# Optimization experiments

Hardware: AMD Instinct MI355X
Metric: run time of the kernel (lower is better)

The kernel has to match this reference:

```python
import jax, jax.numpy as jnp
import numpy as np

N_NODES = 100000
N_EDGES = 1600000
IN_DIM, HID_DIM, OUT_DIM = 512, 64, 32


def _gcn_conv(x, row, col, W, b, n):
    # GCNConv: h = x W; out[v] = sum_{(u,v)} norm(u,v) * h[u] + b
    # deg computed on destination (col) with self-loops already included.
    deg = jax.ops.segment_sum(jnp.ones_like(col, dtype=x.dtype), col, num_segments=n)
    dinv = jnp.where(deg > 0, jax.lax.rsqrt(deg), 0.0)
    norm = dinv[row] * dinv[col]                      # [E]
    h = x @ W                                          # [N, out]
    msg = h[row] * norm[:, None]                       # [E, out] gather
    out = jax.ops.segment_sum(msg, col, num_segments=n)  # scatter-add
    return out + b


def setup_inputs() -> dict:
    key = jax.random.key(0)
    k1, k2, k3, k4 = jax.random.split(key, 4)
    x = jax.random.normal(k1, (N_NODES, IN_DIM), dtype=jnp.float32)
    edge_index = jax.random.randint(k2, (2, N_EDGES), 0, N_NODES, dtype=jnp.int64)
    W1 = jax.random.normal(k3, (IN_DIM, HID_DIM), dtype=jnp.float32) / np.sqrt(IN_DIM)
    b1 = jnp.zeros((HID_DIM,), dtype=jnp.float32)
    W2 = jax.random.normal(k4, (HID_DIM, OUT_DIM), dtype=jnp.float32) / np.sqrt(HID_DIM)
    b2 = jnp.zeros((OUT_DIM,), dtype=jnp.float32)
    return {"x": x, "edge_index": edge_index, "W1": W1, "b1": b1, "W2": W2, "b2": b2}


def reference(x, edge_index, W1, b1, W2, b2):
    n = x.shape[0]
    # add self-loops (PyG GCNConv default add_self_loops=True)
    loop = jnp.arange(n, dtype=edge_index.dtype)
    row = jnp.concatenate([edge_index[0], loop])
    col = jnp.concatenate([edge_index[1], loop])
    h = _gcn_conv(x, row, col, W1, b1, n)
    h = jax.nn.relu(h)
    # dropout is identity in eval mode (training=False)
    h = _gcn_conv(h, row, col, W2, b2, n)
    return jax.nn.log_softmax(h, axis=1)
```

## Files before the change

kernel.cpp:

```cpp
#include <hip/hip_runtime.h>
#include <hip/hip_fp16.h>


#define IN_DIM 512
#define HID    64
#define OUTD   32

typedef __attribute__((ext_vector_type(8))) short bf16x8;
typedef __attribute__((ext_vector_type(4))) float floatx4;
typedef __attribute__((ext_vector_type(4))) unsigned short ushort4v;
typedef __attribute__((ext_vector_type(8))) unsigned short ushort8v;

__device__ __forceinline__ unsigned short f2bf(float f) {
    unsigned int u = __float_as_uint(f);
    unsigned int r = (u + 0x7fffu + ((u >> 16) & 1u)) >> 16;
    return (unsigned short)r;
}
__device__ __forceinline__ float bf2f(unsigned short h) {
    return __uint_as_float(((unsigned int)h) << 16);
}

__device__ __forceinline__ int eidx(const int* idx32, long long e, int is64) {
    if (is64) { const long long* p = (const long long*)idx32; return (int)p[e]; }
    return idx32[e];
}

__global__ void k_init(const float* __restrict__ W1,
                       unsigned short* __restrict__ W1t_hi,
                       unsigned short* __restrict__ W1t_lo,
                       const int* __restrict__ idx, int* __restrict__ flag,
                       int* __restrict__ cnt, int N) {
    int t = blockIdx.x * blockDim.x + threadIdx.x;
    if (t == 0) {
        int z = (idx[1] == 0) & (idx[3] == 0) & (idx[5] == 0) & (idx[7] == 0);
        *flag = z;
    }
    if (t < N) cnt[t] = 0;
    if (t < 64 * 512) {
        int n = t >> 9, k = t & 511;
        float v = W1[k * HID + n];
        unsigned short h = f2bf(v);
        W1t_hi[t] = h;
        W1t_lo[t] = f2bf(v - bf2f(h));
    }
}

__global__ void k_count(const int* __restrict__ idx, const int* __restrict__ flag,
                        int* __restrict__ cnt, int E) {
    int e = blockIdx.x * blockDim.x + threadIdx.x;
    if (e >= E) return;
    const int is64 = *flag;
    int c = eidx(idx, (long long)E + e, is64);
    atomicAdd(&cnt[c], 1);
}

__global__ void k_scanA(const int* __restrict__ cnt, int* __restrict__ rowptr,
                        int* __restrict__ part, float* __restrict__ dinv, int N) {
    __shared__ int s[256];
    const int t = threadIdx.x;
    const int i = blockIdx.x * 256 + t;
    int v = (i < N) ? cnt[i] : 0;
    if (i < N) dinv[i] = rsqrtf((float)(1 + v));
    s[t] = v;
    __syncthreads();
#pragma unroll
    for (int off = 1; off < 256; off <<= 1) {
        int x = (t >= off) ? s[t - off] : 0;
        __syncthreads();
        s[t] += x;
        __syncthreads();
    }
    if (i < N) rowptr[i] = s[t] - v;
    if (t == 255) part[blockIdx.x] = s[255];
}

__global__ void k_scanB(const int* __restrict__ part, int* __restrict__ partex, int nb) {
    __shared__ int s[1024];
    const int t = threadIdx.x;
    int v = (t < nb) ? part[t] : 0;
    s[t] = v;
    __syncthreads();
#pragma unroll
    for (int off = 1; off < 1024; off <<= 1) {
        int x = (t >= off) ? s[t - off] : 0;
        __syncthreads();
        s[t] += x;
        __syncthreads();
    }
    partex[t] = s[t] - v;
}

__global__ void k_scanC(int* __restrict__ rowptr, const int* __restrict__ partex,
                        int N, int E) {
    const int i = blockIdx.x * blockDim.x + threadIdx.x;
    if (i < N) rowptr[i] += partex[i >> 8];
    if (i == 0) rowptr[N] = E;
}

__global__ void k_place(const int* __restrict__ idx, const int* __restrict__ flag,
                        int* __restrict__ cnt, const int* __restrict__ rowptr,
                        int* __restrict__ src, int E) {
    int e = blockIdx.x * blockDim.x + threadIdx.x;
    if (e >= E) return;
    const int is64 = *flag;
    int r = eidx(idx, e, is64);
    int c = eidx(idx, (long long)E + e, is64);
    int ofs = atomicAdd(&cnt[c], -1) - 1;
    src[rowptr[c] + ofs] = r;
}

__launch_bounds__(256)
__global__ void k_gemm1_mfma(const float* __restrict__ x,
                             const unsigned short* __restrict__ Wt_hi,
                             const unsigned short* __restrict__ Wt_lo,
                             const float* __restrict__ dinv,
                             __half* __restrict__ g1, int N) {
    __shared__ unsigned short xs_hi[64 * 72];
    __shared__ unsigned short xs_lo[64 * 72];
    __shared__ unsigned short ws_hi[64 * 72];
    __shared__ unsigned short ws_lo[64 * 72];

    const int t = threadIdx.x;
    const int lane = t & 63;
    const int w = t >> 6;
    const int m = lane & 15;
    const int quad = lane >> 4;
    const int row_base = blockIdx.x * 64;

    const floatx4 zero = {0.0f, 0.0f, 0.0f, 0.0f};
    floatx4 acc[4] = {zero, zero, zero, zero};

    for (int kc = 0; kc < IN_DIM; kc += 64) {
        {
            const int kq = (t & 15) * 4;
#pragma unroll
            for (int p = 0; p < 4; ++p) {
                int rl = (t >> 4) + p * 16;
                int row = row_base + rl;
                if (row > N - 1) row = N - 1;
                float4 v = *(const float4*)(x + (size_t)row * IN_DIM + kc + kq);
                ushort4v hi, lo;
                hi.x = f2bf(v.x); lo.x = f2bf(v.x - bf2f(hi.x));
                hi.y = f2bf(v.y); lo.y = f2bf(v.y - bf2f(hi.y));
                hi.z = f2bf(v.z); lo.z = f2bf(v.z - bf2f(hi.z));
                hi.w = f2bf(v.w); lo.w = f2bf(v.w - bf2f(hi.w));
                *(ushort4v*)&xs_hi[rl * 72 + kq] = hi;
                *(ushort4v*)&xs_lo[rl * 72 + kq] = lo;
            }
        }
        {
            const int nl = t >> 2;
            const int q = (t & 3) * 16;
            const unsigned short* ph = Wt_hi + (size_t)nl * IN_DIM + kc + q;
            const unsigned short* pl = Wt_lo + (size_t)nl * IN_DIM + kc + q;
            *(ushort8v*)&ws_hi[nl * 72 + q]     = *(const ushort8v*)(ph);
            *(ushort8v*)&ws_hi[nl * 72 + q + 8] = *(const ushort8v*)(ph + 8);
            *(ushort8v*)&ws_lo[nl * 72 + q]     = *(const ushort8v*)(pl);
            *(ushort8v*)&ws_lo[nl * 72 + q + 8] = *(const ushort8v*)(pl + 8);
        }
        __syncthreads();
#pragma unroll
        for (int ks = 0; ks < 2; ++ks) {
            const int ko = ks * 32 + quad * 8;
            bf16x8 a_hi = *(const bf16x8*)&xs_hi[(w * 16 + m) * 72 + ko];
            bf16x8 a_lo = *(const bf16x8*)&xs_lo[(w * 16 + m) * 72 + ko];
#pragma unroll
            for (int nt = 0; nt < 4; ++nt) {
                bf16x8 b_hi = *(const bf16x8*)&ws_hi[(nt * 16 + m) * 72 + ko];
                bf16x8 b_lo = *(const bf16x8*)&ws_lo[(nt * 16 + m) * 72 + ko];
                acc[nt] = __builtin_amdgcn_mfma_f32_16x16x32_bf16(a_hi, b_hi, acc[nt], 0, 0, 0);
                acc[nt] = __builtin_amdgcn_mfma_f32_16x16x32_bf16(a_lo, b_hi, acc[nt], 0, 0, 0);
                acc[nt] = __builtin_amdgcn_mfma_f32_16x16x32_bf16(a_hi, b_lo, acc[nt], 0, 0, 0);
            }
        }
        __syncthreads();
    }
#pragma unroll
    for (int r = 0; r < 4; ++r) {
        const int row = row_base + w * 16 + quad * 4 + r;
        if (row < N) {
            const float dv = dinv[row];
#pragma unroll
            for (int nt = 0; nt < 4; ++nt)
                g1[(size_t)row * HID + nt * 16 + m] = __float2half(acc[nt][r] * dv);
        }
    }
}

__launch_bounds__(256)
__global__ void k_agg1_gemm2(const int* __restrict__ rowptr, const int* __restrict__ src,
                             const __half* __restrict__ g1, const float* __restrict__ W2,
                             const float* __restrict__ b1, const float* __restrict__ dinv,
                             __half* __restrict__ g2, int N) {
    __shared__ float w2s[HID * OUTD];
    __shared__ float hs[4][HID];

    const int t = threadIdx.x;
    for (int i = t; i < HID * OUTD; i += 256) w2s[i] = W2[i];

    const int w = t >> 6, lane = t & 63;
    const int v = blockIdx.x * 4 + w;
    float dv = 0.0f;
    if (v < N) {
        float acc = (float)g1[(size_t)v * HID + lane];
        int i = rowptr[v];
        const int end = rowptr[v + 1];
        for (; i + 3 < end; i += 4) {
            int r0 = src[i], r1 = src[i + 1], r2 = src[i + 2], r3 = src[i + 3];
            float a0 = (float)g1[(size_t)r0 * HID + lane];
            float a1 = (float)g1[(size_t)r1 * HID + lane];
            float a2 = (float)g1[(size_t)r2 * HID + lane];
            float a3 = (float)g1[(size_t)r3 * HID + lane];
            acc += (a0 + a1) + (a2 + a3);
        }
        for (; i < end; ++i) acc += (float)g1[(size_t)src[i] * HID + lane];
        dv = dinv[v];
        hs[w][lane] = fmaxf(fmaf(dv, acc, b1[lane]), 0.0f);
    }
    __syncthreads();
    if (v < N) {
        const int j = lane & 31, half = lane >> 5;
        float s = 0.0f;
#pragma unroll
        for (int k = 0; k < 32; ++k) {
            const int kk = half * 32 + k;
            s = fmaf(hs[w][kk], w2s[kk * OUTD + j], s);
        }
        s += __shfl_down(s, 32);
        if (lane < 32) g2[(size_t)v * OUTD + j] = __float2half(s * dv);
    }
}

__global__ void k_out(const int* __restrict__ rowptr, const int* __restrict__ src,
                      const __half* __restrict__ g2, const float* __restrict__ b2,
                      const float* __restrict__ dinv, float* __restrict__ out, int N) {
    const int v = blockIdx.x * 8 + (int)(threadIdx.x >> 5);
    const int j = threadIdx.x & 31;
    if (v >= N) return;
    float acc = (float)g2[(size_t)v * OUTD + j];
    int i = rowptr[v];
    const int end = rowptr[v + 1];
    for (; i + 3 < end; i += 4) {
        int r0 = src[i], r1 = src[i + 1], r2 = src[i + 2], r3 = src[i + 3];
        float a0 = (float)g2[(size_t)r0 * OUTD + j];
        float a1 = (float)g2[(size_t)r1 * OUTD + j];
        float a2 = (float)g2[(size_t)r2 * OUTD + j];
        float a3 = (float)g2[(size_t)r3 * OUTD + j];
        acc += (a0 + a1) + (a2 + a3);
    }
    for (; i < end; ++i) acc += (float)g2[(size_t)src[i] * OUTD + j];
    const float z = fmaf(dinv[v], acc, b2[j]);
    float m = z;
#pragma unroll
    for (int d = 16; d; d >>= 1) m = fmaxf(m, __shfl_xor(m, d, 32));
    float s = expf(z - m);
#pragma unroll
    for (int d = 16; d; d >>= 1) s += __shfl_xor(s, d, 32);
    out[(size_t)v * OUTD + j] = z - m - logf(s);
}

extern "C" void kernel_launch(void* const* d_in, const int* in_sizes, int n_in,
                              void* d_out, int out_size, void* d_ws, size_t ws_size,
                              hipStream_t stream) {
    const float* x   = (const float*)d_in[0];
    const int*   idx = (const int*)d_in[1];
    const float* W1  = (const float*)d_in[2];
    const float* b1  = (const float*)d_in[3];
    const float* W2  = (const float*)d_in[4];
    const float* b2  = (const float*)d_in[5];
    float* out = (float*)d_out;

    const int N = in_sizes[0] / IN_DIM;
    const int E = in_sizes[1] / 2;

    unsigned short* W1t_hi = (unsigned short*)d_ws;
    unsigned short* W1t_lo = W1t_hi + 64 * 512;
    int* cnt    = (int*)(W1t_lo + 64 * 512);
    int* rowptr = cnt + N;
    int* part   = rowptr + (N + 4);
    int* partex = part + 1024;
    int* srcA   = partex + 1024;
    int* flag   = srcA + E;
    float* dinv = (float*)(flag + 4);
    __half* g1  = (__half*)(dinv + N);
    __half* g2  = g1 + (size_t)N * HID;

    const int B = 256;
    const int nb = (N + 255) / 256;

    k_init<<<(N + B - 1) / B, B, 0, stream>>>(W1, W1t_hi, W1t_lo, idx, flag, cnt, N);
    k_count<<<(E + B - 1) / B, B, 0, stream>>>(idx, flag, cnt, E);
    k_scanA<<<nb, 256, 0, stream>>>(cnt, rowptr, part, dinv, N);
    k_scanB<<<1, 1024, 0, stream>>>(part, partex, nb);
    k_scanC<<<nb, 256, 0, stream>>>(rowptr, partex, N, E);
    k_place<<<(E + B - 1) / B, B, 0, stream>>>(idx, flag, cnt, rowptr, srcA, E);

    k_gemm1_mfma<<<(N + 63) / 64, 256, 0, stream>>>(x, W1t_hi, W1t_lo, dinv, g1, N);
    k_agg1_gemm2<<<(N + 3) / 4, 256, 0, stream>>>(rowptr, srcA, g1, W2, b1, dinv, g2, N);
    k_out<<<(N + 7) / 8, B, 0, stream>>>(rowptr, srcA, g2, b2, dinv, out, N);
}
```

Baseline: 592.3 us.

## Vectorize gather aggregation with 4-wide half loads and more nodes per block

```diff
diff --git a/kernel.cpp b/kernel.cpp
--- a/kernel.cpp
+++ b/kernel.cpp
@@ -18,6 +18,13 @@
 }
 __device__ __forceinline__ float bf2f(unsigned short h) {
     return __uint_as_float(((unsigned int)h) << 16);
+}
+
+__device__ __forceinline__ float4 ld4h(const __half* p) {
+    uint2 u = *(const uint2*)(p);
+    __half2 a = *(__half2*)&u.x, b = *(__half2*)&u.y;
+    float2 fa = __half22float2(a), fb = __half22float2(b);
+    return make_float4(fa.x, fa.y, fb.x, fb.y);
 }
 
 __device__ __forceinline__ int eidx(const int* idx32, long long e, int is64) {
@@ -193,70 +200,110 @@
                              const float* __restrict__ b1, const float* __restrict__ dinv,
                              __half* __restrict__ g2, int N) {
     __shared__ float w2s[HID * OUTD];
-    __shared__ float hs[4][HID];
+    __shared__ float hs[16][HID];
+    __shared__ float sdv[16];
 
     const int t = threadIdx.x;
     for (int i = t; i < HID * OUTD; i += 256) w2s[i] = W2[i];
 
-    const int w = t >> 6, lane = t & 63;
-    const int v = blockIdx.x * 4 + w;
-    float dv = 0.0f;
+    const int wv = t >> 6, lane = t & 63;
+    const int grp = lane >> 4;
+    const int l16 = lane & 15;
+    const int vl = wv * 4 + grp;
+    const int v = blockIdx.x * 16 + vl;
+    const int c0 = l16 * 4;
+
     if (v < N) {
-        float acc = (float)g1[(size_t)v * HID + lane];
+        float4 acc = ld4h(g1 + (size_t)v * HID + c0);
         int i = rowptr[v];
         const int end = rowptr[v + 1];
         for (; i + 3 < end; i += 4) {
             int r0 = src[i], r1 = src[i + 1], r2 = src[i + 2], r3 = src[i + 3];
-            float a0 = (float)g1[(size_t)r0 * HID + lane];
-            float a1 = (float)g1[(size_t)r1 * HID + lane];
-            float a2 = (float)g1[(size_t)r2 * HID + lane];
-            float a3 = (float)g1[(size_t)r3 * HID + lane];
-            acc += (a0 + a1) + (a2 + a3);
-        }
-        for (; i < end; ++i) acc += (float)g1[(size_t)src[i] * HID + lane];
-        dv = dinv[v];
-        hs[w][lane] = fmaxf(fmaf(dv, acc, b1[lane]), 0.0f);
+            float4 a0 = ld4h(g1 + (size_t)r0 * HID + c0);
+            float4 a1 = ld4h(g1 + (size_t)r1 * HID + c0);
+            float4 a2 = ld4h(g1 + (size_t)r2 * HID + c0);
+            float4 a3 = ld4h(g1 + (size_t)r3 * HID + c0);
+            acc.x += (a0.x + a1.x) + (a2.x + a3.x);
+            acc.y += (a0.y + a1.y) + (a2.y + a3.y);
+            acc.z += (a0.z + a1.z) + (a2.z + a3.z);
+            acc.w += (a0.w + a1.w) + (a2.w + a3.w);
+        }
+        for (; i < end; ++i) {
+            float4 a = ld4h(g1 + (size_t)src[i] * HID + c0);
+            acc.x += a.x; acc.y += a.y; acc.z += a.z; acc.w += a.w;
+        }
+        const float dv = dinv[v];
+        const float4 b = *(const float4*)(b1 + c0);
+        float4 h;
+        h.x = fmaxf(fmaf(dv, acc.x, b.x), 0.0f);
+        h.y = fmaxf(fmaf(dv, acc.y, b.y), 0.0f);
+        h.z = fmaxf(fmaf(dv, acc.z, b.z), 0.0f);
+        h.w = fmaxf(fmaf(dv, acc.w, b.w), 0.0f);
+        *(float4*)&hs[vl][c0] = h;
+        if (l16 == 0) sdv[vl] = dv;
     }
     __syncthreads();
-    if (v < N) {
-        const int j = lane & 31, half = lane >> 5;
-        float s = 0.0f;
-#pragma unroll
-        for (int k = 0; k < 32; ++k) {
-            const int kk = half * 32 + k;
-            s = fmaf(hs[w][kk], w2s[kk * OUTD + j], s);
-        }
-        s += __shfl_down(s, 32);
-        if (lane < 32) g2[(size_t)v * OUTD + j] = __float2half(s * dv);
+#pragma unroll
+    for (int hh = 0; hh < 2; ++hh) {
+        const int o = hh * 256 + t;
+        const int vert = o >> 5;
+        const int j = o & 31;
+        const int gv = blockIdx.x * 16 + vert;
+        if (gv < N) {
+            float s = 0.0f;
+#pragma unroll
+            for (int k = 0; k < HID; ++k) s = fmaf(hs[vert][k], w2s[k * OUTD + j], s);
+            g2[(size_t)gv * OUTD + j] = __float2half(s * sdv[vert]);
+        }
     }
 }
 
 __global__ void k_out(const int* __restrict__ rowptr, const int* __restrict__ src,
                       const __half* __restrict__ g2, const float* __restrict__ b2,
                       const float* __restrict__ dinv, float* __restrict__ out, int N) {
-    const int v = blockIdx.x * 8 + (int)(threadIdx.x >> 5);
-    const int j = threadIdx.x & 31;
+    const int t = threadIdx.x;
+    const int wv = t >> 6, lane = t & 63;
+    const int grp = lane >> 3;
+    const int l8 = lane & 7;
+    const int v = blockIdx.x * 32 + wv * 8 + grp;
     if (v >= N) return;
-    float acc = (float)g2[(size_t)v * OUTD + j];
+    const int c0 = l8 * 4;
+
+    float4 acc = ld4h(g2 + (size_t)v * OUTD + c0);
     int i = rowptr[v];
     const int end = rowptr[v + 1];
     for (; i + 3 < end; i += 4) {
         int r0 = src[i], r1 = src[i + 1], r2 = src[i + 2], r3 = src[i + 3];
-        float a0 = (float)g2[(size_t)r0 * OUTD + j];
-        float a1 = (float)g2[(size_t)r1 * OUTD + j];
-        float a2 = (float)g2[(size_t)r2 * OUTD + j];
-        float a3 = (float)g2[(size_t)r3 * OUTD + j];
-        acc += (a0 + a1) + (a2 + a3);
-    }
-    for (; i < end; ++i) acc += (float)g2[(size_t)src[i] * OUTD + j];
-    const float z = fmaf(dinv[v], acc, b2[j]);
-    float m = z;
-#pragma unroll
-    for (int d = 16; d; d >>= 1) m = fmaxf(m, __shfl_xor(m, d, 32));
-    float s = expf(z - m);
-#pragma unroll
-    for (int d = 16; d; d >>= 1) s += __shfl_xor(s, d, 32);
-    out[(size_t)v * OUTD + j] = z - m - logf(s);
+        float4 a0 = ld4h(g2 + (size_t)r0 * OUTD + c0);
+        float4 a1 = ld4h(g2 + (size_t)r1 * OUTD + c0);
+        float4 a2 = ld4h(g2 + (size_t)r2 * OUTD + c0);
+        float4 a3 = ld4h(g2 + (size_t)r3 * OUTD + c0);
+        acc.x += (a0.x + a1.x) + (a2.x + a3.x);
+        acc.y += (a0.y + a1.y) + (a2.y + a3.y);
+        acc.z += (a0.z + a1.z) + (a2.z + a3.z);
+        acc.w += (a0.w + a1.w) + (a2.w + a3.w);
+    }
+    for (; i < end; ++i) {
+        float4 a = ld4h(g2 + (size_t)src[i] * OUTD + c0);
+        acc.x += a.x; acc.y += a.y; acc.z += a.z; acc.w += a.w;
+    }
+    const float dv = dinv[v];
+    const float4 b = *(const float4*)(b2 + c0);
+    float4 z;
+    z.x = fmaf(dv, acc.x, b.x);
+    z.y = fmaf(dv, acc.y, b.y);
+    z.z = fmaf(dv, acc.z, b.z);
+    z.w = fmaf(dv, acc.w, b.w);
+    float m = fmaxf(fmaxf(z.x, z.y), fmaxf(z.z, z.w));
+#pragma unroll
+    for (int d = 1; d < 8; d <<= 1) m = fmaxf(m, __shfl_xor(m, d, 64));
+    float s = expf(z.x - m) + expf(z.y - m) + expf(z.z - m) + expf(z.w - m);
+#pragma unroll
+    for (int d = 1; d < 8; d <<= 1) s += __shfl_xor(s, d, 64);
+    const float ml = m + logf(s);
+    float4 o;
+    o.x = z.x - ml; o.y = z.y - ml; o.z = z.z - ml; o.w = z.w - ml;
+    *(float4*)(out + (size_t)v * OUTD + c0) = o;
 }
 
 extern "C" void kernel_launch(void* const* d_in, const int* in_sizes, int n_in,
@@ -296,6 +343,6 @@
     k_place<<<(E + B - 1) / B, B, 0, stream>>>(idx, flag, cnt, rowptr, srcA, E);
 
     k_gemm1_mfma<<<(N + 63) / 64, 256, 0, stream>>>(x, W1t_hi, W1t_lo, dinv, g1, N);
-    k_agg1_gemm2<<<(N + 3) / 4, 256, 0, stream>>>(rowptr, srcA, g1, W2, b1, dinv, g2, N);
-    k_out<<<(N + 7) / 8, B, 0, stream>>>(rowptr, srcA, g2, b2, dinv, out, N);
-}
+    k_agg1_gemm2<<<(N + 15) / 16, 256, 0, stream>>>(rowptr, srcA, g1, W2, b1, dinv, g2, N);
+    k_out<<<(N + 31) / 32, B, 0, stream>>>(rowptr, srcA, g2, b2, dinv, out, N);
+}
```

Result: faster. 547.5 us (-7.6%).
